# Kernel tuning notes

Measured on AMD Instinct MI355X. Metric: run time of the kernel, lower is better.

## Reference

```python
import jax, jax.numpy as jnp
import numpy as np

NEG = -9e15

def setup_inputs() -> dict:
    key = jax.random.key(0)
    k1, k2, k3, k4 = jax.random.split(key, 4)
    N, Fin, Fout = 8192, 256, 256
    h = jax.random.normal(k1, (N, Fin), dtype=jnp.float32)
    adj = jax.random.randint(k2, (N, N), 0, 2).astype(jnp.float32)
    W = jax.random.normal(k3, (Fin, Fout), dtype=jnp.float32) * (1.414 * np.sqrt(2.0 / (Fin + Fout)))
    a = jax.random.normal(k4, (2 * Fout, 1), dtype=jnp.float32) * (1.414 * np.sqrt(2.0 / (2 * Fout + 1)))
    return {"h": h, "adj": adj, "W": W, "a": a}

def reference(h, adj, W, a):
    Fout = W.shape[1]
    Wh = h @ W                                  # [N, Fout]
    Wh1 = Wh @ a[:Fout, :]                      # [N, 1]
    Wh2 = Wh @ a[Fout:, :]                      # [N, 1]
    e = jax.nn.leaky_relu(Wh1 + Wh2.T, 0.2)     # [N, N]
    mask = (adj > 0).astype(e.dtype)
    e = e * mask + NEG * (1.0 - mask)
    attention = jax.nn.softmax(e, axis=1)       # [N, N]
    h_prime = attention @ Wh                    # [N, Fout]
    return jax.nn.elu(h_prime)
```

## Files before the change

kernel.cpp:

```cpp
#include <hip/hip_runtime.h>
#include <hip/hip_bf16.h>
#include <stdint.h>

typedef __attribute__((ext_vector_type(4))) short short4v;
typedef __attribute__((ext_vector_type(8))) short short8v;
typedef __attribute__((ext_vector_type(4))) float float4v;

#define NN 8192
#define FIN 256
#define FOUT 256

__device__ __forceinline__ short f2bf(float f) {
    unsigned u = __float_as_uint(f);
    unsigned r = u + 0x7fffu + ((u >> 16) & 1u);
    return (short)(r >> 16);
}

__global__ __launch_bounds__(256) void k_wt(const float* __restrict__ W, short* __restrict__ WT) {
    int k = blockIdx.x, n = threadIdx.x;
    WT[n * 256 + k] = f2bf(W[k * 256 + n]);
}

__global__ __launch_bounds__(256) void k_gemm1(const float* __restrict__ h, const short* __restrict__ WT,
                                               float* __restrict__ Wh) {
    __shared__ short sA[64 * 40];
    __shared__ short sB[64 * 40];
    int bm = blockIdx.x;
    int bn = blockIdx.y;
    int t  = threadIdx.x;
    int w = t >> 6, lane = t & 63, quad = lane >> 4, l16 = lane & 15;

    float4v acc[4];
#pragma unroll
    for (int c = 0; c < 4; c++)
#pragma unroll
        for (int j = 0; j < 4; j++) acc[c][j] = 0.f;

    int r  = t >> 2;
    int ko = (t & 3) * 8;

    for (int k0 = 0; k0 < 256; k0 += 32) {
        const float4v* src = (const float4v*)&h[(size_t)(64 * bm + r) * 256 + k0 + ko];
        float4v v0 = src[0], v1 = src[1];
        short8v pk;
        pk[0] = f2bf(v0[0]); pk[1] = f2bf(v0[1]); pk[2] = f2bf(v0[2]); pk[3] = f2bf(v0[3]);
        pk[4] = f2bf(v1[0]); pk[5] = f2bf(v1[1]); pk[6] = f2bf(v1[2]); pk[7] = f2bf(v1[3]);
        *(short8v*)&sA[r * 40 + ko] = pk;
        short8v bv = *(const short8v*)&WT[(size_t)(64 * bn + r) * 256 + k0 + ko];
        *(short8v*)&sB[r * 40 + ko] = bv;
        __syncthreads();

        short8v af = *(const short8v*)&sA[(16 * w + l16) * 40 + quad * 8];
#pragma unroll
        for (int c = 0; c < 4; c++) {
            short8v bf = *(const short8v*)&sB[(16 * c + l16) * 40 + quad * 8];
            acc[c] = __builtin_amdgcn_mfma_f32_16x16x32_bf16(af, bf, acc[c], 0, 0, 0);
        }
        __syncthreads();
    }
#pragma unroll
    for (int c = 0; c < 4; c++)
#pragma unroll
        for (int j = 0; j < 4; j++) {
            int row = 64 * bm + 16 * w + quad * 4 + j;
            int col = 64 * bn + 16 * c + l16;
            Wh[(size_t)row * 256 + col] = acc[c][j];
        }
}

__global__ __launch_bounds__(256) void k_rowstats(const float* __restrict__ Wh, const float* __restrict__ a,
                                                  float* __restrict__ Wh1, float* __restrict__ Wh2,
                                                  unsigned* __restrict__ maxenc) {
    int w = threadIdx.x >> 6, lane = threadIdx.x & 63;
    int row = blockIdx.x * 4 + w;
    float s1 = 0.f, s2 = 0.f;
#pragma unroll
    for (int j = 0; j < 4; j++) {
        int c = lane + 64 * j;
        float v = Wh[(size_t)row * 256 + c];
        s1 += v * a[c];
        s2 += v * a[256 + c];
    }
#pragma unroll
    for (int off = 32; off; off >>= 1) {
        s1 += __shfl_down(s1, off);
        s2 += __shfl_down(s2, off);
    }
    if (lane == 0) {
        Wh1[row] = s1;
        Wh2[row] = s2;
        unsigned u = __float_as_uint(s2);
        unsigned key = (u & 0x80000000u) ? ~u : (u | 0x80000000u);
        atomicMax(maxenc, key);
    }
}

__global__ __launch_bounds__(256) void k_transpose(const float* __restrict__ Wh, short* __restrict__ WhT) {
    __shared__ short sT[64 * 72];
    int bm = blockIdx.x, bn = blockIdx.y;
    int t = threadIdx.x;
#pragma unroll
    for (int i = 0; i < 4; i++) {
        int idx = i * 256 + t;
        int r = idx >> 4, c4 = (idx & 15) * 4;
        float4v v = *(const float4v*)&Wh[(size_t)(64 * bm + r) * 256 + 64 * bn + c4];
#pragma unroll
        for (int j = 0; j < 4; j++) sT[(c4 + j) * 72 + r] = f2bf(v[j]);
    }
    __syncthreads();
    int c = t >> 2, ro = (t & 3) * 16;
#pragma unroll
    for (int hh = 0; hh < 2; hh++) {
        short8v v = *(const short8v*)&sT[c * 72 + ro + 8 * hh];
        *(short8v*)&WhT[(size_t)(64 * bn + c) * 8192 + 64 * bm + ro + 8 * hh] = v;
    }
}

__global__ __launch_bounds__(512, 4) void k_gat(const float* __restrict__ adj, const short* __restrict__ WhT,
                                                const float* __restrict__ Wh1, const float* __restrict__ Wh2,
                                                const unsigned* __restrict__ maxenc,
                                                float* __restrict__ Cacc, float* __restrict__ Lacc,
                                                int Ksub) {
    __shared__ short sB[256 * 64];
    __shared__ short sA[64 * 72];
    int bm = blockIdx.x;
    int sidx = blockIdx.y;
    int kb = sidx * Ksub;
    int t = threadIdx.x;
    int lane = t & 63, quad = lane >> 4, l16 = lane & 15;
    int w = t >> 6;
    int mr = (w >> 2) * 32;
    int cg = w & 3;

    unsigned key = maxenc[0];
    unsigned u = (key & 0x80000000u) ? (key & 0x7fffffffu) : ~key;
    float maxw2 = __uint_as_float(u);

    int r  = t >> 3;
    int kc = (t & 7) * 8;
    float wh1r = Wh1[64 * bm + r];
    float sup = wh1r + maxw2;
    float ci = fmaxf(sup, 0.2f * sup);

    const float* adj_row = &adj[(size_t)(64 * bm + r) * 8192 + kb];
    const float* w2base  = &Wh2[kb];

    int schunk = (t & 7) ^ ((t >> 3) & 7);
    const short* gb0 = &WhT[(size_t)(t >> 3) * 8192 + kb + schunk * 8];
    short* lb0 = &sB[t * 8];

    float4v acc[2][4];
#pragma unroll
    for (int rt = 0; rt < 2; rt++)
#pragma unroll
        for (int c = 0; c < 4; c++)
#pragma unroll
            for (int j = 0; j < 4; j++) acc[rt][c][j] = 0.f;
    float lsum = 0.f;

    float4v av0 = *(const float4v*)&adj_row[kc];
    float4v av1 = *(const float4v*)&adj_row[kc + 4];
    float4v w20 = *(const float4v*)&w2base[kc];
    float4v w21 = *(const float4v*)&w2base[kc + 4];

    for (int k0 = 0; k0 < Ksub; k0 += 64) {
#pragma unroll
        for (int i = 0; i < 4; i++) {
            __builtin_amdgcn_global_load_lds(
                (const __attribute__((address_space(1))) void*)(gb0 + (size_t)i * 64 * 8192 + k0),
                (__attribute__((address_space(3))) void*)(lb0 + i * 512 * 8),
                16, 0, 0);
        }
        short8v pk;
#pragma unroll
        for (int j = 0; j < 4; j++) {
            float s = wh1r + w20[j];
            float f = fmaxf(s, 0.2f * s);
            float p = __expf(f - ci);
            p = (av0[j] > 0.f) ? p : 0.f;
            lsum += p;
            pk[j] = f2bf(p);
        }
#pragma unroll
        for (int j = 0; j < 4; j++) {
            float s = wh1r + w21[j];
            float f = fmaxf(s, 0.2f * s);
            float p = __expf(f - ci);
            p = (av1[j] > 0.f) ? p : 0.f;
            lsum += p;
            pk[4 + j] = f2bf(p);
        }
        *(short8v*)&sA[r * 72 + kc] = pk;
        if (k0 + 64 < Ksub) {
            av0 = *(const float4v*)&adj_row[k0 + 64 + kc];
            av1 = *(const float4v*)&adj_row[k0 + 64 + kc + 4];
            w20 = *(const float4v*)&w2base[k0 + 64 + kc];
            w21 = *(const float4v*)&w2base[k0 + 64 + kc + 4];
        }
        __syncthreads();

#pragma unroll
        for (int kk = 0; kk < 2; kk++) {
            short8v af0 = *(const short8v*)&sA[(mr + l16) * 72 + kk * 32 + quad * 8];
            short8v af1 = *(const short8v*)&sA[(mr + 16 + l16) * 72 + kk * 32 + quad * 8];
#pragma unroll
            for (int c = 0; c < 4; c++) {
                int n = 64 * cg + 16 * c + l16;
                int ch = (kk * 4 + quad) ^ (n & 7);
                short8v bf = *(const short8v*)&sB[n * 64 + ch * 8];
                acc[0][c] = __builtin_amdgcn_mfma_f32_16x16x32_bf16(af0, bf, acc[0][c], 0, 0, 0);
                acc[1][c] = __builtin_amdgcn_mfma_f32_16x16x32_bf16(af1, bf, acc[1][c], 0, 0, 0);
            }
        }
        __syncthreads();
    }

#pragma unroll
    for (int off = 4; off; off >>= 1) lsum += __shfl_xor(lsum, off, 8);
    if ((t & 7) == 0) atomicAdd(&Lacc[64 * bm + r], lsum);

#pragma unroll
    for (int rt = 0; rt < 2; rt++)
#pragma unroll
        for (int c = 0; c < 4; c++)
#pragma unroll
            for (int j = 0; j < 4; j++) {
                int row = 64 * bm + mr + rt * 16 + quad * 4 + j;
                int col = 64 * cg + 16 * c + l16;
                atomicAdd(&Cacc[(size_t)row * 256 + col], acc[rt][c][j]);
            }
}

__global__ __launch_bounds__(256) void k_final(const float* __restrict__ Cacc, const float* __restrict__ Lacc,
                                               float* __restrict__ out) {
    int idx = blockIdx.x * 256 + threadIdx.x;
    int row = idx >> 6;
    int c4 = (idx & 63) * 4;
    float4v v = *(const float4v*)&Cacc[(size_t)row * 256 + c4];
    float inv = 1.0f / fmaxf(Lacc[row], 1e-30f);
    float4v o;
#pragma unroll
    for (int j = 0; j < 4; j++) {
        float x = v[j] * inv;
        o[j] = (x > 0.f) ? x : (__expf(x) - 1.f);
    }
    *(float4v*)&out[(size_t)row * 256 + c4] = o;
}

extern "C" void kernel_launch(void* const* d_in, const int* in_sizes, int n_in,
                              void* d_out, int out_size, void* d_ws, size_t ws_size,
                              hipStream_t stream) {
    const float* h   = (const float*)d_in[0];
    const float* adj = (const float*)d_in[1];
    const float* W   = (const float*)d_in[2];
    const float* a   = (const float*)d_in[3];
    float* out = (float*)d_out;

    const int S = 4;
    const int Ksub = NN / S;

    char* ws = (char*)d_ws;
    float*    Wh     = (float*)(ws);
    float*    Cacc   = (float*)(ws);
    short*    WhT    = (short*)(ws + 8388608);
    char*     tail   = ws + 12582912;
    short*    WT     = (short*)(tail);
    float*    Wh1    = (float*)(tail + 131072);
    float*    Wh2    = (float*)(tail + 163840);
    float*    Lacc   = (float*)(tail + 196608);
    unsigned* maxenc = (unsigned*)(tail + 229376);

    hipMemsetAsync(maxenc, 0, sizeof(unsigned), stream);

    k_wt<<<256, 256, 0, stream>>>(W, WT);
    k_gemm1<<<dim3(128, 4), 256, 0, stream>>>(h, WT, Wh);
    k_rowstats<<<2048, 256, 0, stream>>>(Wh, a, Wh1, Wh2, maxenc);
    k_transpose<<<dim3(128, 4), 256, 0, stream>>>(Wh, WhT);
    hipMemsetAsync(Cacc, 0, (size_t)NN * 256 * sizeof(float), stream);
    hipMemsetAsync(Lacc, 0, (size_t)NN * sizeof(float), stream);
    k_gat<<<dim3(128, S), 512, 0, stream>>>(adj, WhT, Wh1, Wh2, maxenc, Cacc, Lacc, Ksub);
    k_final<<<2048, 256, 0, stream>>>(Cacc, Lacc, out);
}
```

Baseline: 542.8 us.

## Double-buffer WhT tile in LDS and prefetch next tile during compute

The B tile (WhT slice) is double-buffered in shared memory, and the next tile's async global-to-LDS loads are issued before the current tile's exp/mask computation and MFMA work. Explicit s_waitcnt vmcnt counts replace __syncthreads so the outstanding prefetch is not drained, and the MFMA section runs at raised wave priority. This is meant to hide global load latency for the B operand, at the cost of doubling LDS use (occupancy risk at 4 blocks per CU) and relying on hand-counted vmcnt values.

```diff
diff --git a/kernel.cpp b/kernel.cpp
--- a/kernel.cpp
+++ b/kernel.cpp
@@ -121,7 +121,7 @@
                                                 const unsigned* __restrict__ maxenc,
                                                 float* __restrict__ Cacc, float* __restrict__ Lacc,
                                                 int Ksub) {
-    __shared__ short sB[256 * 64];
+    __shared__ short sB[2][256 * 64];
     __shared__ short sA[64 * 72];
     int bm = blockIdx.x;
     int sidx = blockIdx.y;
@@ -147,7 +147,7 @@
 
     int schunk = (t & 7) ^ ((t >> 3) & 7);
     const short* gb0 = &WhT[(size_t)(t >> 3) * 8192 + kb + schunk * 8];
-    short* lb0 = &sB[t * 8];
+    short* sBbase = &sB[0][0];
 
     float4v acc[2][4];
 #pragma unroll
@@ -158,47 +158,61 @@
             for (int j = 0; j < 4; j++) acc[rt][c][j] = 0.f;
     float lsum = 0.f;
 
+#pragma unroll
+    for (int i = 0; i < 4; i++)
+        __builtin_amdgcn_global_load_lds(
+            (const __attribute__((address_space(1))) void*)(gb0 + (size_t)i * 64 * 8192),
+            (__attribute__((address_space(3))) void*)(sBbase + t * 8 + i * 512 * 8),
+            16, 0, 0);
     float4v av0 = *(const float4v*)&adj_row[kc];
     float4v av1 = *(const float4v*)&adj_row[kc + 4];
     float4v w20 = *(const float4v*)&w2base[kc];
     float4v w21 = *(const float4v*)&w2base[kc + 4];
-
-    for (int k0 = 0; k0 < Ksub; k0 += 64) {
-#pragma unroll
-        for (int i = 0; i < 4; i++) {
-            __builtin_amdgcn_global_load_lds(
-                (const __attribute__((address_space(1))) void*)(gb0 + (size_t)i * 64 * 8192 + k0),
-                (__attribute__((address_space(3))) void*)(lb0 + i * 512 * 8),
-                16, 0, 0);
+    float4v bv0, bv1, x20, x21;
+
+    auto body = [&](int k0, int curbuf,
+                    float4v& AV0, float4v& AV1, float4v& W20, float4v& W21,
+                    float4v& NAV0, float4v& NAV1, float4v& NW20, float4v& NW21) {
+        int k0n = k0 + 64;
+        if (k0n < Ksub) {
+            short* lb = sBbase + (curbuf ^ 1) * (256 * 64) + t * 8;
+            const short* gs = gb0 + k0n;
+#pragma unroll
+            for (int i = 0; i < 4; i++)
+                __builtin_amdgcn_global_load_lds(
+                    (const __attribute__((address_space(1))) void*)(gs + (size_t)i * 64 * 8192),
+                    (__attribute__((address_space(3))) void*)(lb + i * 512 * 8),
+                    16, 0, 0);
+            NAV0 = *(const float4v*)&adj_row[k0n + kc];
+            NAV1 = *(const float4v*)&adj_row[k0n + kc + 4];
+            NW20 = *(const float4v*)&w2base[k0n + kc];
+            NW21 = *(const float4v*)&w2base[k0n + kc + 4];
         }
         short8v pk;
 #pragma unroll
         for (int j = 0; j < 4; j++) {
-            float s = wh1r + w20[j];
+            float s = wh1r + W20[j];
             float f = fmaxf(s, 0.2f * s);
             float p = __expf(f - ci);
-            p = (av0[j] > 0.f) ? p : 0.f;
+            p = (AV0[j] > 0.f) ? p : 0.f;
             lsum += p;
             pk[j] = f2bf(p);
         }
 #pragma unroll
         for (int j = 0; j < 4; j++) {
-            float s = wh1r + w21[j];
+            float s = wh1r + W21[j];
             float f = fmaxf(s, 0.2f * s);
             float p = __expf(f - ci);
-            p = (av1[j] > 0.f) ? p : 0.f;
+            p = (AV1[j] > 0.f) ? p : 0.f;
             lsum += p;
             pk[4 + j] = f2bf(p);
         }
         *(short8v*)&sA[r * 72 + kc] = pk;
-        if (k0 + 64 < Ksub) {
-            av0 = *(const float4v*)&adj_row[k0 + 64 + kc];
-            av1 = *(const float4v*)&adj_row[k0 + 64 + kc + 4];
-            w20 = *(const float4v*)&w2base[k0 + 64 + kc];
-            w21 = *(const float4v*)&w2base[k0 + 64 + kc + 4];
-        }
-        __syncthreads();
-
+        if (k0n < Ksub) asm volatile("s_waitcnt vmcnt(8) lgkmcnt(0)" ::: "memory");
+        else            asm volatile("s_waitcnt vmcnt(0) lgkmcnt(0)" ::: "memory");
+        __builtin_amdgcn_s_barrier();
+        __builtin_amdgcn_s_setprio(1);
+        const short* sBc = sBbase + curbuf * (256 * 64);
 #pragma unroll
         for (int kk = 0; kk < 2; kk++) {
             short8v af0 = *(const short8v*)&sA[(mr + l16) * 72 + kk * 32 + quad * 8];
@@ -207,12 +221,18 @@
             for (int c = 0; c < 4; c++) {
                 int n = 64 * cg + 16 * c + l16;
                 int ch = (kk * 4 + quad) ^ (n & 7);
-                short8v bf = *(const short8v*)&sB[n * 64 + ch * 8];
+                short8v bf = *(const short8v*)&sBc[n * 64 + ch * 8];
                 acc[0][c] = __builtin_amdgcn_mfma_f32_16x16x32_bf16(af0, bf, acc[0][c], 0, 0, 0);
                 acc[1][c] = __builtin_amdgcn_mfma_f32_16x16x32_bf16(af1, bf, acc[1][c], 0, 0, 0);
             }
         }
-        __syncthreads();
+        __builtin_amdgcn_s_setprio(0);
+        __builtin_amdgcn_s_barrier();
+    };
+
+    for (int k0 = 0; k0 < Ksub; k0 += 128) {
+        body(k0,      0, av0, av1, w20, w21, bv0, bv1, x20, x21);
+        body(k0 + 64, 1, bv0, bv1, x20, x21, av0, av1, w20, w21);
     }
 
 #pragma unroll
```

Measured after the change: 541.0 us. No clear change (-0.3%).

## Double-buffer WhT tile through registers with prefetch two stages ahead

Applied to the files above, without the earlier changes.

Replaces the direct global-to-LDS async loads of the WhT tile with register-staged loads into a double-buffered shared array. Loads run two K-steps ahead and are written to the alternate buffer while the current one feeds MFMA. Raw s_barrier plus waitcnt replaces __syncthreads, and s_setprio raises wave priority around the MFMA block. This doubles sB to 64 KB and adds vector registers, which may lower occupancy under the 512-thread, 4-block launch bound. The K loop now steps by 128, which assumes Ksub is a multiple of 128.

```diff
diff --git a/kernel.cpp b/kernel.cpp
--- a/kernel.cpp
+++ b/kernel.cpp
@@ -121,7 +121,7 @@
                                                 const unsigned* __restrict__ maxenc,
                                                 float* __restrict__ Cacc, float* __restrict__ Lacc,
                                                 int Ksub) {
-    __shared__ short sB[256 * 64];
+    __shared__ short sB[2][256 * 64];
     __shared__ short sA[64 * 72];
     int bm = blockIdx.x;
     int sidx = blockIdx.y;
@@ -145,9 +145,14 @@
     const float* adj_row = &adj[(size_t)(64 * bm + r) * 8192 + kb];
     const float* w2base  = &Wh2[kb];
 
-    int schunk = (t & 7) ^ ((t >> 3) & 7);
-    const short* gb0 = &WhT[(size_t)(t >> 3) * 8192 + kb + schunk * 8];
-    short* lb0 = &sB[t * 8];
+    int nrow = t >> 1;
+    int half = t & 1;
+    const short* gB = &WhT[(size_t)nrow * 8192 + kb + half * 32];
+    int nx = nrow & 7;
+    int sbw0 = nrow * 64 + (((half * 4 + 0) ^ nx)) * 8;
+    int sbw1 = nrow * 64 + (((half * 4 + 1) ^ nx)) * 8;
+    int sbw2 = nrow * 64 + (((half * 4 + 2) ^ nx)) * 8;
+    int sbw3 = nrow * 64 + (((half * 4 + 3) ^ nx)) * 8;
 
     float4v acc[2][4];
 #pragma unroll
@@ -158,62 +163,97 @@
             for (int j = 0; j < 4; j++) acc[rt][c][j] = 0.f;
     float lsum = 0.f;
 
-    float4v av0 = *(const float4v*)&adj_row[kc];
-    float4v av1 = *(const float4v*)&adj_row[kc + 4];
-    float4v w20 = *(const float4v*)&w2base[kc];
-    float4v w21 = *(const float4v*)&w2base[kc + 4];
-
-    for (int k0 = 0; k0 < Ksub; k0 += 64) {
-#pragma unroll
-        for (int i = 0; i < 4; i++) {
-            __builtin_amdgcn_global_load_lds(
-                (const __attribute__((address_space(1))) void*)(gb0 + (size_t)i * 64 * 8192 + k0),
-                (__attribute__((address_space(3))) void*)(lb0 + i * 512 * 8),
-                16, 0, 0);
-        }
-        short8v pk;
-#pragma unroll
-        for (int j = 0; j < 4; j++) {
-            float s = wh1r + w20[j];
-            float f = fmaxf(s, 0.2f * s);
-            float p = __expf(f - ci);
-            p = (av0[j] > 0.f) ? p : 0.f;
-            lsum += p;
-            pk[j] = f2bf(p);
-        }
-#pragma unroll
-        for (int j = 0; j < 4; j++) {
-            float s = wh1r + w21[j];
-            float f = fmaxf(s, 0.2f * s);
-            float p = __expf(f - ci);
-            p = (av1[j] > 0.f) ? p : 0.f;
-            lsum += p;
-            pk[4 + j] = f2bf(p);
-        }
-        *(short8v*)&sA[r * 72 + kc] = pk;
-        if (k0 + 64 < Ksub) {
-            av0 = *(const float4v*)&adj_row[k0 + 64 + kc];
-            av1 = *(const float4v*)&adj_row[k0 + 64 + kc + 4];
-            w20 = *(const float4v*)&w2base[k0 + 64 + kc];
-            w21 = *(const float4v*)&w2base[k0 + 64 + kc + 4];
-        }
-        __syncthreads();
-
-#pragma unroll
-        for (int kk = 0; kk < 2; kk++) {
-            short8v af0 = *(const short8v*)&sA[(mr + l16) * 72 + kk * 32 + quad * 8];
-            short8v af1 = *(const short8v*)&sA[(mr + 16 + l16) * 72 + kk * 32 + quad * 8];
-#pragma unroll
-            for (int c = 0; c < 4; c++) {
-                int n = 64 * cg + 16 * c + l16;
-                int ch = (kk * 4 + quad) ^ (n & 7);
-                short8v bf = *(const short8v*)&sB[n * 64 + ch * 8];
-                acc[0][c] = __builtin_amdgcn_mfma_f32_16x16x32_bf16(af0, bf, acc[0][c], 0, 0, 0);
-                acc[1][c] = __builtin_amdgcn_mfma_f32_16x16x32_bf16(af1, bf, acc[1][c], 0, 0, 0);
-            }
-        }
-        __syncthreads();
-    }
+    short8v a0, a1, a2, a3;
+    short8v b0, b1, b2, b3;
+    float4v av0, av1, w20, w21;
+    float4v cv0, cv1, x20, x21;
+
+    av0 = *(const float4v*)&adj_row[kc];
+    av1 = *(const float4v*)&adj_row[kc + 4];
+    w20 = *(const float4v*)&w2base[kc];
+    w21 = *(const float4v*)&w2base[kc + 4];
+    a0 = *(const short8v*)&gB[0];
+    a1 = *(const short8v*)&gB[8];
+    a2 = *(const short8v*)&gB[16];
+    a3 = *(const short8v*)&gB[24];
+    *(short8v*)&sB[0][sbw0] = a0;
+    *(short8v*)&sB[0][sbw1] = a1;
+    *(short8v*)&sB[0][sbw2] = a2;
+    *(short8v*)&sB[0][sbw3] = a3;
+    b0 = *(const short8v*)&gB[64];
+    b1 = *(const short8v*)&gB[64 + 8];
+    b2 = *(const short8v*)&gB[64 + 16];
+    b3 = *(const short8v*)&gB[64 + 24];
+
+#define STAGE(K0, CUR, C0, C1, C2, C3, N0, N1, N2, N3, AV0, AV1, AW0, AW1, NV0, NV1, NW0, NW1)   \
+    {                                                                                            \
+        int k1 = (K0) + 64, k2 = (K0) + 128;                                                     \
+        if (k1 < Ksub) {                                                                         \
+            NV0 = *(const float4v*)&adj_row[k1 + kc];                                            \
+            NV1 = *(const float4v*)&adj_row[k1 + kc + 4];                                        \
+            NW0 = *(const float4v*)&w2base[k1 + kc];                                             \
+            NW1 = *(const float4v*)&w2base[k1 + kc + 4];                                         \
+        }                                                                                        \
+        if (k2 < Ksub) {                                                                         \
+            N0 = *(const short8v*)&gB[k2];                                                       \
+            N1 = *(const short8v*)&gB[k2 + 8];                                                   \
+            N2 = *(const short8v*)&gB[k2 + 16];                                                  \
+            N3 = *(const short8v*)&gB[k2 + 24];                                                  \
+        }                                                                                        \
+        if (k1 < Ksub) {                                                                         \
+            *(short8v*)&sB[(CUR) ^ 1][sbw0] = C0;                                                \
+            *(short8v*)&sB[(CUR) ^ 1][sbw1] = C1;                                                \
+            *(short8v*)&sB[(CUR) ^ 1][sbw2] = C2;                                                \
+            *(short8v*)&sB[(CUR) ^ 1][sbw3] = C3;                                                \
+        }                                                                                        \
+        short8v pk;                                                                              \
+        _Pragma("unroll")                                                                        \
+        for (int j = 0; j < 4; j++) {                                                            \
+            float s = wh1r + AW0[j];                                                             \
+            float f = fmaxf(s, 0.2f * s);                                                        \
+            float p = __expf(f - ci);                                                            \
+            p = (AV0[j] > 0.f) ? p : 0.f;                                                        \
+            lsum += p;                                                                           \
+            pk[j] = f2bf(p);                                                                     \
+        }                                                                                        \
+        _Pragma("unroll")                                                                        \
+        for (int j = 0; j < 4; j++) {                                                            \
+            float s = wh1r + AW1[j];                                                             \
+            float f = fmaxf(s, 0.2f * s);                                                        \
+            float p = __expf(f - ci);                                                            \
+            p = (AV1[j] > 0.f) ? p : 0.f;                                                        \
+            lsum += p;                                                                           \
+            pk[4 + j] = f2bf(p);                                                                 \
+        }                                                                                        \
+        *(short8v*)&sA[r * 72 + kc] = pk;                                                        \
+        asm volatile("s_waitcnt lgkmcnt(0)" ::: "memory");                                       \
+        __builtin_amdgcn_s_barrier();                                                            \
+        __builtin_amdgcn_s_setprio(1);                                                           \
+        {                                                                                        \
+            const short* sBc = &sB[(CUR)][0];                                                    \
+            _Pragma("unroll")                                                                    \
+            for (int kk = 0; kk < 2; kk++) {                                                     \
+                short8v af0 = *(const short8v*)&sA[(mr + l16) * 72 + kk * 32 + quad * 8];        \
+                short8v af1 = *(const short8v*)&sA[(mr + 16 + l16) * 72 + kk * 32 + quad * 8];   \
+                _Pragma("unroll")                                                                \
+                for (int c = 0; c < 4; c++) {                                                    \
+                    int n = 64 * cg + 16 * c + l16;                                              \
+                    int ch = (kk * 4 + quad) ^ (n & 7);                                          \
+                    short8v bf = *(const short8v*)&sBc[n * 64 + ch * 8];                         \
+                    acc[0][c] = __builtin_amdgcn_mfma_f32_16x16x32_bf16(af0, bf, acc[0][c], 0, 0, 0); \
+                    acc[1][c] = __builtin_amdgcn_mfma_f32_16x16x32_bf16(af1, bf, acc[1][c], 0, 0, 0); \
+                }                                                                                \
+            }                                                                                    \
+        }                                                                                        \
+        __builtin_amdgcn_s_setprio(0);                                                           \
+        __builtin_amdgcn_s_barrier();                                                            \
+    }
+
+    for (int k0 = 0; k0 < Ksub; k0 += 128) {
+        STAGE(k0,      0, b0, b1, b2, b3, a0, a1, a2, a3, av0, av1, w20, w21, cv0, cv1, x20, x21)
+        STAGE(k0 + 64, 1, a0, a1, a2, a3, b0, b1, b2, b3, cv0, cv1, x20, x21, av0, av1, w20, w21)
+    }
+#undef STAGE
 
 #pragma unroll
     for (int off = 4; off; off >>= 1) lsum += __shfl_xor(lsum, off, 8);
```

Measured after the change: 691.2 us. 27.3% more time.
